# Optimization experiments

Hardware: AMD Instinct MI355X
Metric: run time of the kernel (lower is better)

Reference implementation:

```python
import jax, jax.numpy as jnp
import numpy as np

B, S, H, I, E, K = 4, 2048, 1024, 4096, 8, 2


def setup_inputs() -> dict:
    key = jax.random.key(0)
    ks = jax.random.split(key, 5)
    scale = 1.0 / np.sqrt(H)
    return {
        "hidden_states": jax.random.normal(ks[0], (B, S, H), dtype=jnp.float32),
        "router_w": jax.random.normal(ks[1], (E, H), dtype=jnp.float32) * scale,
        "gate_w": jax.random.normal(ks[2], (E, I, H), dtype=jnp.float32) * scale,
        "up_w": jax.random.normal(ks[3], (E, I, H), dtype=jnp.float32) * scale,
        "down_w": jax.random.normal(ks[4], (E, H, I), dtype=jnp.float32) * (1.0 / np.sqrt(I)),
        "top_k": K,
    }


def reference(hidden_states, router_w, gate_w, up_w, down_w, top_k):
    # Router: logits -> softmax -> top-k -> renormalized weights (eval mode, no jitter)
    logits = jnp.einsum("bsh,eh->bse", hidden_states, router_w)
    probs = jax.nn.softmax(logits, axis=-1)
    expert_weights, expert_indices = jax.lax.top_k(probs, top_k)  # [B,S,K]
    expert_weights = expert_weights / expert_weights.sum(axis=-1, keepdims=True)

    n_experts = router_w.shape[0]
    # Per-token combine weight for each expert: [B,S,E]
    combine = (jax.nn.one_hot(expert_indices, n_experts, dtype=expert_weights.dtype)
               * expert_weights[..., None]).sum(axis=-2)

    out = jnp.zeros_like(hidden_states)
    for e in range(n_experts):  # fixed small expert count
        g = jax.nn.silu(hidden_states @ gate_w[e].T)  # [B,S,I]
        u = hidden_states @ up_w[e].T                 # [B,S,I]
        y = (g * u) @ down_w[e].T                     # [B,S,H]
        out = out + combine[..., e:e + 1] * y
    return out
```

## Files before the change

### kernel.cpp

```cpp
#include <hip/hip_runtime.h>
#include <hip/hip_bf16.h>
#include <math.h>
#include <stdint.h>

#define TOKENS 8192
#define HD 1024
#define ID 4096
#define NE 8
#define RMAX 17408
#define MAXT 136

typedef __attribute__((ext_vector_type(8))) short short8v;
typedef __attribute__((ext_vector_type(4))) float f32x4;

typedef const __attribute__((address_space(1))) unsigned int* gas_u32p;
typedef __attribute__((address_space(3))) unsigned int* las_u32p;

__device__ __forceinline__ void stage16(const void* g, void* l) {
  __builtin_amdgcn_global_load_lds((gas_u32p)g, (las_u32p)l, 16, 0, 0);
}

__global__ __launch_bounds__(256) void convert_kernel(const float* __restrict__ src,
                                                      __hip_bfloat16* __restrict__ dst) {
  size_t i = ((size_t)blockIdx.x * 256 + threadIdx.x) * 8;
  float4 a = ((const float4*)(src + i))[0];
  float4 b = ((const float4*)(src + i))[1];
  union { __hip_bfloat16 h[8]; int4 v; } u;
  u.h[0] = __float2bfloat16(a.x); u.h[1] = __float2bfloat16(a.y);
  u.h[2] = __float2bfloat16(a.z); u.h[3] = __float2bfloat16(a.w);
  u.h[4] = __float2bfloat16(b.x); u.h[5] = __float2bfloat16(b.y);
  u.h[6] = __float2bfloat16(b.z); u.h[7] = __float2bfloat16(b.w);
  *(int4*)(dst + i) = u.v;
}

__global__ __launch_bounds__(256) void router_kernel(
    const float* __restrict__ h, const float* __restrict__ rw,
    __hip_bfloat16* __restrict__ hx, int* __restrict__ tidx,
    float* __restrict__ tw, int* __restrict__ cnt) {
  int wid = threadIdx.x >> 6, lane = threadIdx.x & 63;
  int t = blockIdx.x * 4 + wid;
  const float4* h4 = (const float4*)(h + (size_t)t * HD);
  float x[16];
  {
    float4 xa = h4[lane * 4 + 0], xb = h4[lane * 4 + 1], xc = h4[lane * 4 + 2], xd = h4[lane * 4 + 3];
    x[0] = xa.x; x[1] = xa.y; x[2] = xa.z; x[3] = xa.w;
    x[4] = xb.x; x[5] = xb.y; x[6] = xb.z; x[7] = xb.w;
    x[8] = xc.x; x[9] = xc.y; x[10] = xc.z; x[11] = xc.w;
    x[12] = xd.x; x[13] = xd.y; x[14] = xd.z; x[15] = xd.w;
  }
  union { __hip_bfloat16 hb[16]; int4 v[2]; } u;
#pragma unroll
  for (int j = 0; j < 16; j++) u.hb[j] = __float2bfloat16(x[j]);
  {
    int4* hxp = (int4*)(hx + (size_t)t * HD + lane * 16);
    hxp[0] = u.v[0]; hxp[1] = u.v[1];
  }
  double acc[NE];
#pragma unroll
  for (int e = 0; e < NE; e++) {
    const float4* w4 = (const float4*)(rw + e * HD);
    float4 wa = w4[lane * 4 + 0], wb = w4[lane * 4 + 1], wc = w4[lane * 4 + 2], wd = w4[lane * 4 + 3];
    double s = 0.0;
    s += (double)x[0] * wa.x + (double)x[1] * wa.y + (double)x[2] * wa.z + (double)x[3] * wa.w;
    s += (double)x[4] * wb.x + (double)x[5] * wb.y + (double)x[6] * wb.z + (double)x[7] * wb.w;
    s += (double)x[8] * wc.x + (double)x[9] * wc.y + (double)x[10] * wc.z + (double)x[11] * wc.w;
    s += (double)x[12] * wd.x + (double)x[13] * wd.y + (double)x[14] * wd.z + (double)x[15] * wd.w;
    acc[e] = s;
  }
#pragma unroll
  for (int off = 32; off >= 1; off >>= 1)
#pragma unroll
    for (int e = 0; e < NE; e++) acc[e] += __shfl_xor(acc[e], off, 64);
  if (lane == 0) {
    int i0 = 0; double l0 = acc[0];
#pragma unroll
    for (int e = 1; e < NE; e++) if (acc[e] > l0) { l0 = acc[e]; i0 = e; }
    int i1 = -1; double l1 = -1.0e300;
#pragma unroll
    for (int e = 0; e < NE; e++) if (e != i0 && acc[e] > l1) { l1 = acc[e]; i1 = e; }
    double r = exp(l1 - l0);
    float w0 = (float)(1.0 / (1.0 + r));
    float w1 = (float)(r / (1.0 + r));
    tidx[t * 2 + 0] = i0; tidx[t * 2 + 1] = i1;
    tw[t * 2 + 0] = w0;  tw[t * 2 + 1] = w1;
    atomicAdd(&cnt[i0], 1); atomicAdd(&cnt[i1], 1);
  }
}

__global__ void scan_kernel(const int* __restrict__ cnt, int* __restrict__ ofs, int* __restrict__ cnt2) {
  if (threadIdx.x == 0) {
    int a = 0;
    for (int e = 0; e < NE; e++) { ofs[e] = a; a += (cnt[e] + 127) & ~127; }
    ofs[NE] = a;
  }
  if (threadIdx.x < NE) cnt2[threadIdx.x] = 0;
}

__global__ __launch_bounds__(256) void scatter_kernel(
    const int* __restrict__ tidx, const float* __restrict__ tw,
    const int* __restrict__ ofs, int* __restrict__ cnt2,
    int* __restrict__ rowmap, int* __restrict__ slots) {
  int t = blockIdx.x * 256 + threadIdx.x;
#pragma unroll
  for (int k = 0; k < 2; k++) {
    int e = tidx[t * 2 + k];
    int pos = atomicAdd(&cnt2[e], 1);
    int row = ofs[e] + pos;
    rowmap[row] = t;
    slots[t * 2 + k] = row;
  }
}

__global__ __launch_bounds__(256) void gather_kernel(
    const __hip_bfloat16* __restrict__ hx, const int* __restrict__ rowmap,
    const int* __restrict__ ofs, __hip_bfloat16* __restrict__ A1) {
  int r = blockIdx.x * 4 + (threadIdx.x >> 6);
  int lane = threadIdx.x & 63;
  if (r >= ofs[NE]) return;
  int t = rowmap[r];
  int4* dst = (int4*)(A1 + (size_t)r * HD);
  if (t < 0) {
    int4 z = {0, 0, 0, 0};
    dst[lane * 2 + 0] = z; dst[lane * 2 + 1] = z;
  } else {
    const int4* src = (const int4*)(hx + (size_t)t * HD);
    dst[lane * 2 + 0] = src[lane * 2 + 0];
    dst[lane * 2 + 1] = src[lane * 2 + 1];
  }
}

__global__ __launch_bounds__(256, 2) void gemm1_kernel(
    const __hip_bfloat16* __restrict__ A1, const __hip_bfloat16* __restrict__ Wg,
    const __hip_bfloat16* __restrict__ Wu, const int* __restrict__ ofs,
    __hip_bfloat16* __restrict__ act) {
  __shared__ __hip_bfloat16 sA[128 * 64];
  __shared__ __hip_bfloat16 sG[128 * 64];
  __shared__ __hip_bfloat16 sU[128 * 64];
  const int tm = blockIdx.x, tn = blockIdx.y;
  const int Rtot = ofs[NE];
  const int row0 = tm * 128;
  if (row0 >= Rtot) return;
  int e = 0;
#pragma unroll
  for (int i = 1; i < NE; i++) e += (row0 >= ofs[i]);
  const int t = threadIdx.x, wid = t >> 6, lane = t & 63;
  const int wm = wid >> 1, wn = wid & 1;
  const int fr = lane & 15, fk = (lane >> 4) << 3;

  const char* gA = (const char*)(A1 + (size_t)row0 * HD);
  const char* gG = (const char*)(Wg + ((size_t)e * ID + tn * 128) * HD);
  const char* gU = (const char*)(Wu + ((size_t)e * ID + tn * 128) * HD);

  int srow[4], scol[4];
#pragma unroll
  for (int i = 0; i < 4; i++) { int li = (i * 256 + t) * 16; srow[i] = li >> 7; scol[i] = li & 127; }

  f32x4 accG[4][4], accU[4][4];
#pragma unroll
  for (int m = 0; m < 4; m++)
#pragma unroll
    for (int n = 0; n < 4; n++) { accG[m][n] = (f32x4)(0.0f); accU[m][n] = (f32x4)(0.0f); }

  for (int kt = 0; kt < HD / 64; kt++) {
    const int kb = kt * 128;
#pragma unroll
    for (int i = 0; i < 4; i++) {
      size_t go = (size_t)srow[i] * 2048 + kb + scol[i];
      stage16(gA + go, (char*)sA + i * 4096 + wid * 1024);
      stage16(gG + go, (char*)sG + i * 4096 + wid * 1024);
      stage16(gU + go, (char*)sU + i * 4096 + wid * 1024);
    }
    __syncthreads();
#pragma unroll
    for (int kk = 0; kk < 64; kk += 32) {
      short8v av[4], bg[4], bu[4];
#pragma unroll
      for (int m = 0; m < 4; m++)
        av[m] = *(const short8v*)(sA + (wm * 64 + m * 16 + fr) * 64 + kk + fk);
#pragma unroll
      for (int n = 0; n < 4; n++) {
        bg[n] = *(const short8v*)(sG + (wn * 64 + n * 16 + fr) * 64 + kk + fk);
        bu[n] = *(const short8v*)(sU + (wn * 64 + n * 16 + fr) * 64 + kk + fk);
      }
#pragma unroll
      for (int m = 0; m < 4; m++)
#pragma unroll
        for (int n = 0; n < 4; n++) {
          accG[m][n] = __builtin_amdgcn_mfma_f32_16x16x32_bf16(av[m], bg[n], accG[m][n], 0, 0, 0);
          accU[m][n] = __builtin_amdgcn_mfma_f32_16x16x32_bf16(av[m], bu[n], accU[m][n], 0, 0, 0);
        }
    }
    __syncthreads();
  }
  const int rb = row0 + wm * 64 + ((lane >> 4) << 2);
  const int cb = tn * 128 + wn * 64 + fr;
#pragma unroll
  for (int m = 0; m < 4; m++)
#pragma unroll
    for (int i = 0; i < 4; i++) {
      int r = rb + m * 16 + i;
      __hip_bfloat16* dst = act + (size_t)r * ID + cb;
#pragma unroll
      for (int n = 0; n < 4; n++) {
        float g = accG[m][n][i], uu = accU[m][n][i];
        float s = g / (1.0f + __expf(-g));
        dst[n * 16] = __float2bfloat16(s * uu);
      }
    }
}

__global__ __launch_bounds__(256, 2) void gemm2_kernel(
    const __hip_bfloat16* __restrict__ act, const __hip_bfloat16* __restrict__ Wd,
    const int* __restrict__ ofs, float* __restrict__ ybuf) {
  __shared__ __hip_bfloat16 sA[128 * 64];
  __shared__ __hip_bfloat16 sB[128 * 64];
  const int tm = blockIdx.x, tn = blockIdx.y;
  const int Rtot = ofs[NE];
  const int row0 = tm * 128;
  if (row0 >= Rtot) return;
  int e = 0;
#pragma unroll
  for (int i = 1; i < NE; i++) e += (row0 >= ofs[i]);
  const int t = threadIdx.x, wid = t >> 6, lane = t & 63;
  const int wm = wid >> 1, wn = wid & 1;
  const int fr = lane & 15, fk = (lane >> 4) << 3;

  const char* gA = (const char*)(act + (size_t)row0 * ID);
  const char* gB = (const char*)(Wd + ((size_t)e * HD + tn * 128) * ID);

  int srow[4], scol[4];
#pragma unroll
  for (int i = 0; i < 4; i++) { int li = (i * 256 + t) * 16; srow[i] = li >> 7; scol[i] = li & 127; }

  f32x4 acc[4][4];
#pragma unroll
  for (int m = 0; m < 4; m++)
#pragma unroll
    for (int n = 0; n < 4; n++) acc[m][n] = (f32x4)(0.0f);

  for (int kt = 0; kt < ID / 64; kt++) {
    const int kb = kt * 128;
#pragma unroll
    for (int i = 0; i < 4; i++) {
      size_t go = (size_t)srow[i] * 8192 + kb + scol[i];
      stage16(gA + go, (char*)sA + i * 4096 + wid * 1024);
      stage16(gB + go, (char*)sB + i * 4096 + wid * 1024);
    }
    __syncthreads();
#pragma unroll
    for (int kk = 0; kk < 64; kk += 32) {
      short8v av[4], bv[4];
#pragma unroll
      for (int m = 0; m < 4; m++)
        av[m] = *(const short8v*)(sA + (wm * 64 + m * 16 + fr) * 64 + kk + fk);
#pragma unroll
      for (int n = 0; n < 4; n++)
        bv[n] = *(const short8v*)(sB + (wn * 64 + n * 16 + fr) * 64 + kk + fk);
#pragma unroll
      for (int m = 0; m < 4; m++)
#pragma unroll
        for (int n = 0; n < 4; n++)
          acc[m][n] = __builtin_amdgcn_mfma_f32_16x16x32_bf16(av[m], bv[n], acc[m][n], 0, 0, 0);
    }
    __syncthreads();
  }
  const int rb = row0 + wm * 64 + ((lane >> 4) << 2);
  const int cb = tn * 128 + wn * 64 + fr;
#pragma unroll
  for (int m = 0; m < 4; m++)
#pragma unroll
    for (int i = 0; i < 4; i++) {
      int r = rb + m * 16 + i;
      float* dst = ybuf + (size_t)r * HD + cb;
#pragma unroll
      for (int n = 0; n < 4; n++) dst[n * 16] = acc[m][n][i];
    }
}

__global__ __launch_bounds__(256) void combine_kernel(
    const float* __restrict__ ybuf, const int* __restrict__ slots,
    const float* __restrict__ tw, float* __restrict__ out) {
  int t = blockIdx.x * 4 + (threadIdx.x >> 6);
  int lane = threadIdx.x & 63;
  int r0 = slots[t * 2 + 0], r1 = slots[t * 2 + 1];
  float w0 = tw[t * 2 + 0], w1 = tw[t * 2 + 1];
  const float4* y0 = (const float4*)(ybuf + (size_t)r0 * HD);
  const float4* y1 = (const float4*)(ybuf + (size_t)r1 * HD);
  float4* o = (float4*)(out + (size_t)t * HD);
#pragma unroll
  for (int j = 0; j < 4; j++) {
    int ix = j * 64 + lane;
    float4 a = y0[ix], b = y1[ix];
    float4 c;
    c.x = w0 * a.x + w1 * b.x; c.y = w0 * a.y + w1 * b.y;
    c.z = w0 * a.z + w1 * b.z; c.w = w0 * a.w + w1 * b.w;
    o[ix] = c;
  }
}

extern "C" void kernel_launch(void* const* d_in, const int* in_sizes, int n_in,
                              void* d_out, int out_size, void* d_ws, size_t ws_size,
                              hipStream_t stream) {
  (void)in_sizes; (void)n_in; (void)out_size; (void)ws_size;
  const float* h  = (const float*)d_in[0];
  const float* rw = (const float*)d_in[1];
  const float* gw = (const float*)d_in[2];
  const float* uw = (const float*)d_in[3];
  const float* dw = (const float*)d_in[4];
  float* out = (float*)d_out;

  char* ws = (char*)d_ws;
  size_t off = 0;
  auto alloc = [&](size_t bytes) { char* p = ws + off; off += (bytes + 255) & ~255ULL; return p; };
  __hip_bfloat16* wg  = (__hip_bfloat16*)alloc((size_t)NE * ID * HD * 2);
  __hip_bfloat16* wu  = (__hip_bfloat16*)alloc((size_t)NE * ID * HD * 2);
  __hip_bfloat16* wd  = (__hip_bfloat16*)alloc((size_t)NE * HD * ID * 2);
  __hip_bfloat16* hx  = (__hip_bfloat16*)alloc((size_t)TOKENS * HD * 2);
  __hip_bfloat16* A1  = (__hip_bfloat16*)alloc((size_t)RMAX * HD * 2);
  __hip_bfloat16* act = (__hip_bfloat16*)alloc((size_t)RMAX * ID * 2);
  float* ybuf = (float*)alloc((size_t)RMAX * HD * 4);
  int* rowmap = (int*)alloc(RMAX * 4);
  int* tidx   = (int*)alloc(TOKENS * 2 * 4);
  float* twt  = (float*)alloc(TOKENS * 2 * 4);
  int* slots  = (int*)alloc(TOKENS * 2 * 4);
  int* cnt    = (int*)alloc(256);
  int* cnt2   = (int*)alloc(256);
  int* ofs    = (int*)alloc(256);

  hipMemsetAsync(cnt, 0, NE * 4, stream);
  hipMemsetAsync(rowmap, 0xFF, RMAX * 4, stream);

  convert_kernel<<<16384, 256, 0, stream>>>(gw, wg);
  convert_kernel<<<16384, 256, 0, stream>>>(uw, wu);
  convert_kernel<<<16384, 256, 0, stream>>>(dw, wd);
  router_kernel<<<TOKENS / 4, 256, 0, stream>>>(h, rw, hx, tidx, twt, cnt);
  scan_kernel<<<1, 64, 0, stream>>>(cnt, ofs, cnt2);
  scatter_kernel<<<TOKENS / 256, 256, 0, stream>>>(tidx, twt, ofs, cnt2, rowmap, slots);
  gather_kernel<<<RMAX / 4, 256, 0, stream>>>(hx, rowmap, ofs, A1);
  dim3 g1(MAXT, ID / 128);
  gemm1_kernel<<<g1, 256, 0, stream>>>(A1, wg, wu, ofs, act);
  dim3 g2(MAXT, HD / 128);
  gemm2_kernel<<<g2, 256, 0, stream>>>(act, wd, ofs, ybuf);
  combine_kernel<<<TOKENS / 4, 256, 0, stream>>>(ybuf, slots, twt, out);
}
```

Baseline: 1.025 ms.

## Rewrite expert GEMMs as 256-row, 8-wave, double-buffered, swizzled-LDS pipelined kernels

Both grouped expert GEMMs move to 512-thread blocks with 256-row tiles (expert padding raised to 256). Operand tiles are double-buffered in 128KB of XOR-swizzled LDS, with async global-to-LDS loads interleaved between MFMA quarter-steps under explicit vmcnt/barrier control and raised MFMA priority. Blocks are remapped across XCDs for locality, and ybuf reuses the hx/A1 workspace. The aim is to hide load latency, cut LDS bank conflicts and raise arithmetic intensity, at the cost of more padding waste and fragile hand-coded wait counts.

```diff
diff --git a/kernel.cpp b/kernel.cpp
--- a/kernel.cpp
+++ b/kernel.cpp
@@ -7,8 +7,8 @@
 #define HD 1024
 #define ID 4096
 #define NE 8
-#define RMAX 17408
-#define MAXT 136
+#define RMAX 18432
+#define MAXT 72
 
 typedef __attribute__((ext_vector_type(8))) short short8v;
 typedef __attribute__((ext_vector_type(4))) float f32x4;
@@ -19,6 +19,12 @@
 __device__ __forceinline__ void stage16(const void* g, void* l) {
   __builtin_amdgcn_global_load_lds((gas_u32p)g, (las_u32p)l, 16, 0, 0);
 }
+
+#define BARRIER asm volatile("s_barrier" ::: "memory")
+#define WAITLGKM asm volatile("s_waitcnt lgkmcnt(0)" ::: "memory")
+#define VMC0 asm volatile("s_waitcnt vmcnt(0)" ::: "memory")
+#define VMC4 asm volatile("s_waitcnt vmcnt(4)" ::: "memory")
+#define VMC6 asm volatile("s_waitcnt vmcnt(6)" ::: "memory")
 
 __global__ __launch_bounds__(256) void convert_kernel(const float* __restrict__ src,
                                                       __hip_bfloat16* __restrict__ dst) {
@@ -90,7 +96,7 @@
 __global__ void scan_kernel(const int* __restrict__ cnt, int* __restrict__ ofs, int* __restrict__ cnt2) {
   if (threadIdx.x == 0) {
     int a = 0;
-    for (int e = 0; e < NE; e++) { ofs[e] = a; a += (cnt[e] + 127) & ~127; }
+    for (int e = 0; e < NE; e++) { ofs[e] = a; a += (cnt[e] + 255) & ~255; }
     ofs[NE] = a;
   }
   if (threadIdx.x < NE) cnt2[threadIdx.x] = 0;
@@ -129,31 +135,62 @@
   }
 }
 
-__global__ __launch_bounds__(256, 2) void gemm1_kernel(
+#define MFMAQ(ACC, MO, NO, AF, BF)                                                         \
+  { _Pragma("unroll") for (int m_ = 0; m_ < 4; m_++)                                       \
+    _Pragma("unroll") for (int n_ = 0; n_ < 2; n_++)                                       \
+    _Pragma("unroll") for (int k_ = 0; k_ < 2; k_++)                                       \
+      ACC[(MO) + m_][(NO) + n_] = __builtin_amdgcn_mfma_f32_16x16x32_bf16(                 \
+          AF[m_][k_], BF[n_][k_], ACC[(MO) + m_][(NO) + n_], 0, 0, 0); }
+
+__global__ __launch_bounds__(512, 2) void gemm1_kernel(
     const __hip_bfloat16* __restrict__ A1, const __hip_bfloat16* __restrict__ Wg,
     const __hip_bfloat16* __restrict__ Wu, const int* __restrict__ ofs,
     __hip_bfloat16* __restrict__ act) {
-  __shared__ __hip_bfloat16 sA[128 * 64];
-  __shared__ __hip_bfloat16 sG[128 * 64];
-  __shared__ __hip_bfloat16 sU[128 * 64];
-  const int tm = blockIdx.x, tn = blockIdx.y;
+  __shared__ __align__(128) char lds[131072];
+  const int nwg = gridDim.x;
+  int wg0 = blockIdx.x;
+  int wg = (wg0 & 7) * (nwg >> 3) + (wg0 >> 3);
+  const int tm = wg >> 5, tn = wg & 31;
   const int Rtot = ofs[NE];
-  const int row0 = tm * 128;
+  const int row0 = tm * 256;
   if (row0 >= Rtot) return;
   int e = 0;
 #pragma unroll
   for (int i = 1; i < NE; i++) e += (row0 >= ofs[i]);
-  const int t = threadIdx.x, wid = t >> 6, lane = t & 63;
+  const int tid = threadIdx.x, wid = tid >> 6, lane = tid & 63;
   const int wm = wid >> 1, wn = wid & 1;
-  const int fr = lane & 15, fk = (lane >> 4) << 3;
-
-  const char* gA = (const char*)(A1 + (size_t)row0 * HD);
-  const char* gG = (const char*)(Wg + ((size_t)e * ID + tn * 128) * HD);
-  const char* gU = (const char*)(Wu + ((size_t)e * ID + tn * 128) * HD);
-
-  int srow[4], scol[4];
-#pragma unroll
-  for (int i = 0; i < 4; i++) { int li = (i * 256 + t) * 16; srow[i] = li >> 7; scol[i] = li & 127; }
+  const int fr = lane & 15, fkE = (lane >> 4) << 3;
+  const int wmB = wm * 64, wnB = wn * 64;
+
+  const char* srcA[4]; const char* srcG[2]; const char* srcU[2];
+  int ldA[4], ldG[2], ldU[2];
+#pragma unroll
+  for (int j = 0; j < 4; j++) {
+    int d = j * 8192 + tid * 16;
+    int row = d >> 7;
+    int kb = (d ^ (((d >> 7) & 7) << 4)) & 127;
+    srcA[j] = (const char*)(A1 + (size_t)(row0 + row) * HD) + kb;
+    ldA[j] = j * 8192 + wid * 1024;
+  }
+#pragma unroll
+  for (int j = 0; j < 2; j++) {
+    int d = j * 8192 + tid * 16;
+    int row = d >> 7;
+    int kb = (d ^ (((d >> 7) & 7) << 4)) & 127;
+    srcG[j] = (const char*)(Wg + ((size_t)e * ID + tn * 128 + row) * HD) + kb;
+    srcU[j] = (const char*)(Wu + ((size_t)e * ID + tn * 128 + row) * HD) + kb;
+    ldG[j] = 32768 + j * 8192 + wid * 1024;
+    ldU[j] = 49152 + j * 8192 + wid * 1024;
+  }
+#define STG_A(j, t, bf) stage16(srcA[j] + (size_t)(t) * 128, (char*)lds + (bf) * 65536 + ldA[j])
+#define STG_G(j, t, bf) stage16(srcG[j] + (size_t)(t) * 128, (char*)lds + (bf) * 65536 + ldG[j])
+#define STG_U(j, t, bf) stage16(srcU[j] + (size_t)(t) * 128, (char*)lds + (bf) * 65536 + ldU[j])
+
+  auto RD = [&](int bf, int poff, int rowi, int kki) -> short8v {
+    int o = ((rowi + fr) << 7) + ((kki << 5) + fkE) * 2;
+    o ^= ((o >> 7) & 7) << 4;
+    return *(const short8v*)(&lds[bf * 65536 + poff + o]);
+  };
 
   f32x4 accG[4][4], accU[4][4];
 #pragma unroll
@@ -161,39 +198,85 @@
 #pragma unroll
     for (int n = 0; n < 4; n++) { accG[m][n] = (f32x4)(0.0f); accU[m][n] = (f32x4)(0.0f); }
 
-  for (int kt = 0; kt < HD / 64; kt++) {
-    const int kb = kt * 128;
-#pragma unroll
-    for (int i = 0; i < 4; i++) {
-      size_t go = (size_t)srow[i] * 2048 + kb + scol[i];
-      stage16(gA + go, (char*)sA + i * 4096 + wid * 1024);
-      stage16(gG + go, (char*)sG + i * 4096 + wid * 1024);
-      stage16(gU + go, (char*)sU + i * 4096 + wid * 1024);
-    }
-    __syncthreads();
-#pragma unroll
-    for (int kk = 0; kk < 64; kk += 32) {
-      short8v av[4], bg[4], bu[4];
-#pragma unroll
-      for (int m = 0; m < 4; m++)
-        av[m] = *(const short8v*)(sA + (wm * 64 + m * 16 + fr) * 64 + kk + fk);
-#pragma unroll
-      for (int n = 0; n < 4; n++) {
-        bg[n] = *(const short8v*)(sG + (wn * 64 + n * 16 + fr) * 64 + kk + fk);
-        bu[n] = *(const short8v*)(sU + (wn * 64 + n * 16 + fr) * 64 + kk + fk);
-      }
-#pragma unroll
-      for (int m = 0; m < 4; m++)
-#pragma unroll
-        for (int n = 0; n < 4; n++) {
-          accG[m][n] = __builtin_amdgcn_mfma_f32_16x16x32_bf16(av[m], bg[n], accG[m][n], 0, 0, 0);
-          accU[m][n] = __builtin_amdgcn_mfma_f32_16x16x32_bf16(av[m], bu[n], accU[m][n], 0, 0, 0);
-        }
-    }
-    __syncthreads();
-  }
-  const int rb = row0 + wm * 64 + ((lane >> 4) << 2);
-  const int cb = tn * 128 + wn * 64 + fr;
+  const int NT = HD / 64;
+#pragma unroll
+  for (int j = 0; j < 4; j++) STG_A(j, 0, 0);
+#pragma unroll
+  for (int j = 0; j < 2; j++) STG_G(j, 0, 0);
+#pragma unroll
+  for (int j = 0; j < 2; j++) STG_U(j, 0, 0);
+#pragma unroll
+  for (int j = 0; j < 4; j++) STG_A(j, 1, 1);
+#pragma unroll
+  for (int j = 0; j < 2; j++) STG_G(j, 1, 1);
+  VMC6; BARRIER;
+
+#pragma unroll 1
+  for (int I = 0; I < NT / 2; ++I) {
+    const int t0 = 2 * I;
+    const bool more = (t0 + 2 < NT);
+    short8v a[4][2], bA[2][2], bB[2][2];
+#pragma unroll
+    for (int m = 0; m < 4; m++) { a[m][0] = RD(0, 0, wmB + m * 16, 0); a[m][1] = RD(0, 0, wmB + m * 16, 1); }
+#pragma unroll
+    for (int n = 0; n < 2; n++) { bA[n][0] = RD(0, 32768, wnB + n * 16, 0); bA[n][1] = RD(0, 32768, wnB + n * 16, 1); }
+    STG_U(0, t0 + 1, 1); STG_U(1, t0 + 1, 1);
+    BARRIER; WAITLGKM;
+    __builtin_amdgcn_s_setprio(1); MFMAQ(accG, 0, 0, a, bA); __builtin_amdgcn_s_setprio(0);
+    BARRIER;
+#pragma unroll
+    for (int n = 0; n < 2; n++) { bB[n][0] = RD(0, 32768, wnB + 32 + n * 16, 0); bB[n][1] = RD(0, 32768, wnB + 32 + n * 16, 1); }
+    if (more) { STG_A(0, t0 + 2, 0); STG_A(1, t0 + 2, 0); }
+    BARRIER; WAITLGKM;
+    __builtin_amdgcn_s_setprio(1); MFMAQ(accG, 0, 2, a, bB); __builtin_amdgcn_s_setprio(0);
+    BARRIER;
+#pragma unroll
+    for (int n = 0; n < 2; n++) { bA[n][0] = RD(0, 49152, wnB + n * 16, 0); bA[n][1] = RD(0, 49152, wnB + n * 16, 1); }
+    if (more) { STG_A(2, t0 + 2, 0); STG_A(3, t0 + 2, 0); }
+    BARRIER; WAITLGKM;
+    __builtin_amdgcn_s_setprio(1); MFMAQ(accU, 0, 0, a, bA); __builtin_amdgcn_s_setprio(0);
+    BARRIER;
+#pragma unroll
+    for (int n = 0; n < 2; n++) { bB[n][0] = RD(0, 49152, wnB + 32 + n * 16, 0); bB[n][1] = RD(0, 49152, wnB + 32 + n * 16, 1); }
+    if (more) { STG_G(0, t0 + 2, 0); STG_G(1, t0 + 2, 0); }
+    BARRIER; WAITLGKM;
+    __builtin_amdgcn_s_setprio(1); MFMAQ(accU, 0, 2, a, bB); __builtin_amdgcn_s_setprio(0);
+    if (more) { VMC6; } else { VMC0; }
+    BARRIER;
+#pragma unroll
+    for (int m = 0; m < 4; m++) { a[m][0] = RD(1, 0, wmB + m * 16, 0); a[m][1] = RD(1, 0, wmB + m * 16, 1); }
+#pragma unroll
+    for (int n = 0; n < 2; n++) { bA[n][0] = RD(1, 32768, wnB + n * 16, 0); bA[n][1] = RD(1, 32768, wnB + n * 16, 1); }
+    if (more) { STG_U(0, t0 + 2, 0); STG_U(1, t0 + 2, 0); }
+    BARRIER; WAITLGKM;
+    __builtin_amdgcn_s_setprio(1); MFMAQ(accG, 0, 0, a, bA); __builtin_amdgcn_s_setprio(0);
+    BARRIER;
+#pragma unroll
+    for (int n = 0; n < 2; n++) { bB[n][0] = RD(1, 32768, wnB + 32 + n * 16, 0); bB[n][1] = RD(1, 32768, wnB + 32 + n * 16, 1); }
+    if (more) { STG_A(0, t0 + 3, 1); STG_A(1, t0 + 3, 1); }
+    BARRIER; WAITLGKM;
+    __builtin_amdgcn_s_setprio(1); MFMAQ(accG, 0, 2, a, bB); __builtin_amdgcn_s_setprio(0);
+    BARRIER;
+#pragma unroll
+    for (int n = 0; n < 2; n++) { bA[n][0] = RD(1, 49152, wnB + n * 16, 0); bA[n][1] = RD(1, 49152, wnB + n * 16, 1); }
+    if (more) { STG_A(2, t0 + 3, 1); STG_A(3, t0 + 3, 1); }
+    BARRIER; WAITLGKM;
+    __builtin_amdgcn_s_setprio(1); MFMAQ(accU, 0, 0, a, bA); __builtin_amdgcn_s_setprio(0);
+    BARRIER;
+#pragma unroll
+    for (int n = 0; n < 2; n++) { bB[n][0] = RD(1, 49152, wnB + 32 + n * 16, 0); bB[n][1] = RD(1, 49152, wnB + 32 + n * 16, 1); }
+    if (more) { STG_G(0, t0 + 3, 1); STG_G(1, t0 + 3, 1); }
+    BARRIER; WAITLGKM;
+    __builtin_amdgcn_s_setprio(1); MFMAQ(accU, 0, 2, a, bB); __builtin_amdgcn_s_setprio(0);
+    if (more) { VMC6; } else { VMC0; }
+    BARRIER;
+  }
+#undef STG_A
+#undef STG_G
+#undef STG_U
+
+  const int rb = row0 + wmB + ((lane >> 4) << 2);
+  const int cb = tn * 128 + wnB + fr;
 #pragma unroll
   for (int m = 0; m < 4; m++)
 #pragma unroll
@@ -209,65 +292,124 @@
     }
 }
 
-__global__ __launch_bounds__(256, 2) void gemm2_kernel(
+__global__ __launch_bounds__(512, 2) void gemm2_kernel(
     const __hip_bfloat16* __restrict__ act, const __hip_bfloat16* __restrict__ Wd,
     const int* __restrict__ ofs, float* __restrict__ ybuf) {
-  __shared__ __hip_bfloat16 sA[128 * 64];
-  __shared__ __hip_bfloat16 sB[128 * 64];
-  const int tm = blockIdx.x, tn = blockIdx.y;
+  __shared__ __align__(128) char lds[131072];
+  const int nwg = gridDim.x;
+  int wg0 = blockIdx.x;
+  int wg = (wg0 & 7) * (nwg >> 3) + (wg0 >> 3);
+  const int tm = wg >> 2, tn = wg & 3;
   const int Rtot = ofs[NE];
-  const int row0 = tm * 128;
+  const int row0 = tm * 256;
   if (row0 >= Rtot) return;
   int e = 0;
 #pragma unroll
   for (int i = 1; i < NE; i++) e += (row0 >= ofs[i]);
-  const int t = threadIdx.x, wid = t >> 6, lane = t & 63;
-  const int wm = wid >> 1, wn = wid & 1;
-  const int fr = lane & 15, fk = (lane >> 4) << 3;
-
-  const char* gA = (const char*)(act + (size_t)row0 * ID);
-  const char* gB = (const char*)(Wd + ((size_t)e * HD + tn * 128) * ID);
-
-  int srow[4], scol[4];
-#pragma unroll
-  for (int i = 0; i < 4; i++) { int li = (i * 256 + t) * 16; srow[i] = li >> 7; scol[i] = li & 127; }
-
-  f32x4 acc[4][4];
-#pragma unroll
-  for (int m = 0; m < 4; m++)
+  const int tid = threadIdx.x, wid = tid >> 6, lane = tid & 63;
+  const int wm = wid >> 2, wn = wid & 3;
+  const int fr = lane & 15, fkE = (lane >> 4) << 3;
+  const int wmB = wm * 128, wnB = wn * 64;
+
+  const char* srcA[4]; const char* srcB[4];
+  int ldA[4], ldB[4];
+#pragma unroll
+  for (int j = 0; j < 4; j++) {
+    int d = j * 8192 + tid * 16;
+    int row = d >> 7;
+    int kb = (d ^ (((d >> 7) & 7) << 4)) & 127;
+    srcA[j] = (const char*)(act + (size_t)(row0 + row) * ID) + kb;
+    srcB[j] = (const char*)(Wd + ((size_t)e * HD + tn * 256 + row) * ID) + kb;
+    ldA[j] = j * 8192 + wid * 1024;
+    ldB[j] = 32768 + j * 8192 + wid * 1024;
+  }
+#define STG_A2(j, t, bf) stage16(srcA[j] + (size_t)(t) * 128, (char*)lds + (bf) * 65536 + ldA[j])
+#define STG_B2(j, t, bf) stage16(srcB[j] + (size_t)(t) * 128, (char*)lds + (bf) * 65536 + ldB[j])
+
+  auto RD = [&](int bf, int poff, int rowi, int kki) -> short8v {
+    int o = ((rowi + fr) << 7) + ((kki << 5) + fkE) * 2;
+    o ^= ((o >> 7) & 7) << 4;
+    return *(const short8v*)(&lds[bf * 65536 + poff + o]);
+  };
+
+  f32x4 acc[8][4];
+#pragma unroll
+  for (int m = 0; m < 8; m++)
 #pragma unroll
     for (int n = 0; n < 4; n++) acc[m][n] = (f32x4)(0.0f);
 
-  for (int kt = 0; kt < ID / 64; kt++) {
-    const int kb = kt * 128;
-#pragma unroll
-    for (int i = 0; i < 4; i++) {
-      size_t go = (size_t)srow[i] * 8192 + kb + scol[i];
-      stage16(gA + go, (char*)sA + i * 4096 + wid * 1024);
-      stage16(gB + go, (char*)sB + i * 4096 + wid * 1024);
-    }
-    __syncthreads();
-#pragma unroll
-    for (int kk = 0; kk < 64; kk += 32) {
-      short8v av[4], bv[4];
-#pragma unroll
-      for (int m = 0; m < 4; m++)
-        av[m] = *(const short8v*)(sA + (wm * 64 + m * 16 + fr) * 64 + kk + fk);
-#pragma unroll
-      for (int n = 0; n < 4; n++)
-        bv[n] = *(const short8v*)(sB + (wn * 64 + n * 16 + fr) * 64 + kk + fk);
-#pragma unroll
-      for (int m = 0; m < 4; m++)
-#pragma unroll
-        for (int n = 0; n < 4; n++)
-          acc[m][n] = __builtin_amdgcn_mfma_f32_16x16x32_bf16(av[m], bv[n], acc[m][n], 0, 0, 0);
-    }
-    __syncthreads();
-  }
-  const int rb = row0 + wm * 64 + ((lane >> 4) << 2);
-  const int cb = tn * 128 + wn * 64 + fr;
-#pragma unroll
-  for (int m = 0; m < 4; m++)
+  const int NT = ID / 64;
+#pragma unroll
+  for (int j = 0; j < 4; j++) STG_B2(j, 0, 0);
+#pragma unroll
+  for (int j = 0; j < 4; j++) STG_A2(j, 0, 0);
+#pragma unroll
+  for (int j = 0; j < 4; j++) STG_B2(j, 1, 1);
+  VMC4; BARRIER;
+
+#pragma unroll 1
+  for (int I = 0; I < NT / 2; ++I) {
+    const int t0 = 2 * I;
+    const bool more = (t0 + 2 < NT);
+    short8v a0[4][2], a1[4][2], b0[2][2], b1[2][2];
+#pragma unroll
+    for (int m = 0; m < 4; m++) { a0[m][0] = RD(0, 0, wmB + m * 16, 0); a0[m][1] = RD(0, 0, wmB + m * 16, 1); }
+#pragma unroll
+    for (int n = 0; n < 2; n++) { b0[n][0] = RD(0, 32768, wnB + n * 16, 0); b0[n][1] = RD(0, 32768, wnB + n * 16, 1); }
+    STG_A2(0, t0 + 1, 1); STG_A2(1, t0 + 1, 1);
+    BARRIER; WAITLGKM;
+    __builtin_amdgcn_s_setprio(1); MFMAQ(acc, 0, 0, a0, b0); __builtin_amdgcn_s_setprio(0);
+    BARRIER;
+#pragma unroll
+    for (int n = 0; n < 2; n++) { b1[n][0] = RD(0, 32768, wnB + 32 + n * 16, 0); b1[n][1] = RD(0, 32768, wnB + 32 + n * 16, 1); }
+    STG_A2(2, t0 + 1, 1); STG_A2(3, t0 + 1, 1);
+    BARRIER; WAITLGKM;
+    __builtin_amdgcn_s_setprio(1); MFMAQ(acc, 0, 2, a0, b1); __builtin_amdgcn_s_setprio(0);
+    BARRIER;
+#pragma unroll
+    for (int m = 0; m < 4; m++) { a1[m][0] = RD(0, 0, wmB + 64 + m * 16, 0); a1[m][1] = RD(0, 0, wmB + 64 + m * 16, 1); }
+    if (more) { STG_B2(0, t0 + 2, 0); STG_B2(1, t0 + 2, 0); }
+    BARRIER; WAITLGKM;
+    __builtin_amdgcn_s_setprio(1); MFMAQ(acc, 4, 2, a1, b1); __builtin_amdgcn_s_setprio(0);
+    BARRIER;
+    if (more) { STG_B2(2, t0 + 2, 0); STG_B2(3, t0 + 2, 0); }
+    BARRIER; WAITLGKM;
+    __builtin_amdgcn_s_setprio(1); MFMAQ(acc, 4, 0, a1, b0); __builtin_amdgcn_s_setprio(0);
+    if (more) { VMC4; } else { VMC0; }
+    BARRIER;
+#pragma unroll
+    for (int m = 0; m < 4; m++) { a0[m][0] = RD(1, 0, wmB + m * 16, 0); a0[m][1] = RD(1, 0, wmB + m * 16, 1); }
+#pragma unroll
+    for (int n = 0; n < 2; n++) { b0[n][0] = RD(1, 32768, wnB + n * 16, 0); b0[n][1] = RD(1, 32768, wnB + n * 16, 1); }
+    if (more) { STG_A2(0, t0 + 2, 0); STG_A2(1, t0 + 2, 0); }
+    BARRIER; WAITLGKM;
+    __builtin_amdgcn_s_setprio(1); MFMAQ(acc, 0, 0, a0, b0); __builtin_amdgcn_s_setprio(0);
+    BARRIER;
+#pragma unroll
+    for (int n = 0; n < 2; n++) { b1[n][0] = RD(1, 32768, wnB + 32 + n * 16, 0); b1[n][1] = RD(1, 32768, wnB + 32 + n * 16, 1); }
+    if (more) { STG_A2(2, t0 + 2, 0); STG_A2(3, t0 + 2, 0); }
+    BARRIER; WAITLGKM;
+    __builtin_amdgcn_s_setprio(1); MFMAQ(acc, 0, 2, a0, b1); __builtin_amdgcn_s_setprio(0);
+    BARRIER;
+#pragma unroll
+    for (int m = 0; m < 4; m++) { a1[m][0] = RD(1, 0, wmB + 64 + m * 16, 0); a1[m][1] = RD(1, 0, wmB + 64 + m * 16, 1); }
+    if (more) { STG_B2(0, t0 + 3, 1); STG_B2(1, t0 + 3, 1); }
+    BARRIER; WAITLGKM;
+    __builtin_amdgcn_s_setprio(1); MFMAQ(acc, 4, 2, a1, b1); __builtin_amdgcn_s_setprio(0);
+    BARRIER;
+    if (more) { STG_B2(2, t0 + 3, 1); STG_B2(3, t0 + 3, 1); }
+    BARRIER; WAITLGKM;
+    __builtin_amdgcn_s_setprio(1); MFMAQ(acc, 4, 0, a1, b0); __builtin_amdgcn_s_setprio(0);
+    if (more) { VMC4; } else { VMC0; }
+    BARRIER;
+  }
+#undef STG_A2
+#undef STG_B2
+
+  const int rb = row0 + wmB + ((lane >> 4) << 2);
+  const int cb = tn * 256 + wnB + fr;
+#pragma unroll
+  for (int m = 0; m < 8; m++)
 #pragma unroll
     for (int i = 0; i < 4; i++) {
       int r = rb + m * 16 + i;
@@ -315,10 +457,15 @@
   __hip_bfloat16* wg  = (__hip_bfloat16*)alloc((size_t)NE * ID * HD * 2);
   __hip_bfloat16* wu  = (__hip_bfloat16*)alloc((size_t)NE * ID * HD * 2);
   __hip_bfloat16* wd  = (__hip_bfloat16*)alloc((size_t)NE * HD * ID * 2);
+  __hip_bfloat16* act = (__hip_bfloat16*)alloc((size_t)RMAX * ID * 2);
+  size_t hx_off = off;
   __hip_bfloat16* hx  = (__hip_bfloat16*)alloc((size_t)TOKENS * HD * 2);
   __hip_bfloat16* A1  = (__hip_bfloat16*)alloc((size_t)RMAX * HD * 2);
-  __hip_bfloat16* act = (__hip_bfloat16*)alloc((size_t)RMAX * ID * 2);
-  float* ybuf = (float*)alloc((size_t)RMAX * HD * 4);
+  float* ybuf = (float*)(ws + hx_off);
+  {
+    size_t yend = hx_off + (size_t)RMAX * HD * 4;
+    if (yend > off) off = (yend + 255) & ~255ULL;
+  }
   int* rowmap = (int*)alloc(RMAX * 4);
   int* tidx   = (int*)alloc(TOKENS * 2 * 4);
   float* twt  = (float*)alloc(TOKENS * 2 * 4);
@@ -337,9 +484,7 @@
   scan_kernel<<<1, 64, 0, stream>>>(cnt, ofs, cnt2);
   scatter_kernel<<<TOKENS / 256, 256, 0, stream>>>(tidx, twt, ofs, cnt2, rowmap, slots);
   gather_kernel<<<RMAX / 4, 256, 0, stream>>>(hx, rowmap, ofs, A1);
-  dim3 g1(MAXT, ID / 128);
-  gemm1_kernel<<<g1, 256, 0, stream>>>(A1, wg, wu, ofs, act);
-  dim3 g2(MAXT, HD / 128);
-  gemm2_kernel<<<g2, 256, 0, stream>>>(act, wd, ofs, ybuf);
+  gemm1_kernel<<<MAXT * 32, 512, 0, stream>>>(A1, wg, wu, ofs, act);
+  gemm2_kernel<<<MAXT * 4, 512, 0, stream>>>(act, wd, ofs, ybuf);
   combine_kernel<<<TOKENS / 4, 256, 0, stream>>>(ybuf, slots, twt, out);
 }
```

After: 925.4 us. 9.7% less time.
